# Kernel optimization log

Measured on AMD Instinct MI355X. Metric: run time of the kernel, lower is better.

Reference implementation:

```python
import jax, jax.numpy as jnp
import numpy as np

B, T, E, S, W, H = 2, 2048, 256, 128, 8, 150

def _mlp(x, w1, b1, w2, b2, w3, b3):
    # Score module: Linear->ReLU->Linear->ReLU->Linear (dropout inactive in eval)
    h = jax.nn.relu(x @ w1 + b1)
    h = jax.nn.relu(h @ w2 + b2)
    return h @ w3 + b3

def _mlp_params(key, d_in):
    k1, k2, k3 = jax.random.split(key, 3)
    s = 0.02
    return (s * jax.random.normal(k1, (d_in, H), jnp.float32), jnp.zeros((H,), jnp.float32),
            s * jax.random.normal(k2, (H, H), jnp.float32), jnp.zeros((H,), jnp.float32),
            s * jax.random.normal(k3, (H, 1), jnp.float32), jnp.zeros((1,), jnp.float32))

def setup_inputs() -> dict:
    key = jax.random.key(0)
    ke, ks, ka, km, kp = jax.random.split(key, 5)
    inp = {
        'batch_embeds': jax.random.normal(ke, (B, T, E), jnp.float32),
        'span_starts': jax.random.randint(ks, (B, S), 0, T - W, jnp.int32),
    }
    for name, k, d in [('attn', ka, E), ('ment', km, 3 * E), ('pair', kp, 9 * E)]:
        w1, b1, w2, b2, w3, b3 = _mlp_params(k, d)
        inp.update({f'{name}_w1': w1, f'{name}_b1': b1, f'{name}_w2': w2,
                    f'{name}_b2': b2, f'{name}_w3': w3, f'{name}_b3': b3})
    return inp

def reference(batch_embeds, span_starts,
              attn_w1, attn_b1, attn_w2, attn_b2, attn_w3, attn_b3,
              ment_w1, ment_b1, ment_w2, ment_b2, ment_w3, ment_b3,
              pair_w1, pair_b1, pair_w2, pair_b2, pair_w3, pair_b3):
    # ---- MentionScore ----
    attns = _mlp(batch_embeds, attn_w1, attn_b1, attn_w2, attn_b2, attn_w3, attn_b3)  # [B,T,1]
    spans = span_starts[:, :, None] + jnp.arange(W)                                   # [B,S,W]
    flat = spans.reshape(B, S * W)
    emb_spans = jnp.take_along_axis(batch_embeds, flat[:, :, None], axis=1).reshape(B, S, W, E)
    attn_spans = jnp.take_along_axis(attns, flat[:, :, None], axis=1).reshape(B, S, W, 1)
    start = emb_spans[:, :, 0, :]
    end = emb_spans[:, :, -1, :]
    weighted = jnp.sum(emb_spans * attn_spans, axis=2)                                # [B,S,E]
    g_i = jnp.concatenate([start, end, weighted], axis=-1)                            # [B,S,3E]
    mention_scores = _mlp(g_i, ment_w1, ment_b1, ment_w2, ment_b2, ment_w3, ment_b3)  # [B,S,1]
    # ---- PairwiseScore: all-pairs cat(g_i, g_j, g_i*g_j) ----
    gi = jnp.broadcast_to(g_i[:, :, None, :], (B, S, S, 3 * E))
    gj = jnp.broadcast_to(g_i[:, None, :, :], (B, S, S, 3 * E))
    pairs = jnp.concatenate([gi, gj, gi * gj], axis=-1)                               # [B,S,S,9E]
    pair_scores = _mlp(pairs, pair_w1, pair_b1, pair_w2, pair_b2, pair_w3, pair_b3)   # [B,S,S,1]
    # extended score = mean(mention_i, mention_j, pair_ij)
    ext = (mention_scores[:, :, None, :] + mention_scores[:, None, :, :] + pair_scores) / 3.0
    return ext
```

## Files before the change

### kernel.cpp

```cpp
#include <hip/hip_runtime.h>
#include <hip/hip_bf16.h>


typedef __bf16 bf16;
typedef __attribute__((ext_vector_type(8))) short v8s;
typedef __attribute__((ext_vector_type(8))) __bf16 v8bf;
typedef __attribute__((ext_vector_type(4))) float v4f;

#define MFMA_BF16(A, B, C) __builtin_amdgcn_mfma_f32_16x16x32_bf16((A), (B), (C), 0, 0, 0)

__device__ __forceinline__ v8bf mul_cvt8(float4 xa, float4 xb, float4 sa, float4 sb) {
    v8bf w;
    w[0] = (bf16)(xa.x * sa.x); w[1] = (bf16)(xa.y * sa.y);
    w[2] = (bf16)(xa.z * sa.z); w[3] = (bf16)(xa.w * sa.w);
    w[4] = (bf16)(xb.x * sb.x); w[5] = (bf16)(xb.y * sb.y);
    w[6] = (bf16)(xb.z * sb.z); w[7] = (bf16)(xb.w * sb.w);
    return w;
}
__device__ __forceinline__ v8bf cvt8(float4 xa, float4 xb) {
    v8bf w;
    w[0] = (bf16)xa.x; w[1] = (bf16)xa.y; w[2] = (bf16)xa.z; w[3] = (bf16)xa.w;
    w[4] = (bf16)xb.x; w[5] = (bf16)xb.y; w[6] = (bf16)xb.z; w[7] = (bf16)xb.w;
    return w;
}

__global__ __launch_bounds__(256) void prep_kernel(
    const float* __restrict__ pw1, const float* __restrict__ pw2,
    const float* __restrict__ aw1, const float* __restrict__ aw2,
    const float* __restrict__ mw1, const float* __restrict__ mw2,
    const float* __restrict__ pb1, const float* __restrict__ pb2, const float* __restrict__ pw3,
    const float* __restrict__ ab1, const float* __restrict__ ab2, const float* __restrict__ aw3,
    const float* __restrict__ mb1, const float* __restrict__ mb2, const float* __restrict__ mw3,
    bf16* __restrict__ w1cT, bf16* __restrict__ w2pT,
    bf16* __restrict__ w1aT, bf16* __restrict__ w2aT, bf16* __restrict__ w2mT,
    bf16* __restrict__ wuvmT, float* __restrict__ bias)
{
    int idx = blockIdx.x * 256 + threadIdx.x;
    if (idx < 147456) {
        int h = idx / 768, e = idx % 768;
        w1cT[idx] = (bf16)((h < 150) ? pw1[(1536 + e) * 150 + h] : 0.f);
    } else if (idx < 178176) {
        int j = idx - 147456; int n = j / 160, k = j % 160;
        w2pT[j] = (bf16)((n < 150 && k < 150) ? pw2[k * 150 + n] : 0.f);
    } else if (idx < 227328) {
        int j = idx - 178176; int h = j / 256, e = j % 256;
        w1aT[j] = (bf16)((h < 150) ? aw1[e * 150 + h] : 0.f);
    } else if (idx < 258048) {
        int j = idx - 227328; int n = j / 160, k = j % 160;
        w2aT[j] = (bf16)((n < 150 && k < 150) ? aw2[k * 150 + n] : 0.f);
    } else if (idx < 288768) {
        int j = idx - 258048; int n = j / 160, k = j % 160;
        w2mT[j] = (bf16)((n < 150 && k < 150) ? mw2[k * 150 + n] : 0.f);
    } else if (idx < 731136) {
        int j = idx - 288768; int s = j / 147456; int r = j % 147456;
        int h = r / 768, e = r % 768;
        float v = 0.f;
        if (h < 150) {
            if (s == 0)      v = pw1[e * 150 + h];
            else if (s == 1) v = pw1[(768 + e) * 150 + h];
            else             v = mw1[e * 150 + h];
        }
        wuvmT[j] = (bf16)v;
    } else if (idx < 732864) {
        int j = idx - 731136; int arr = j / 192, h = j % 192;
        const float* src;
        switch (arr) {
            case 0: src = pb1; break; case 1: src = pb2; break; case 2: src = pw3; break;
            case 3: src = ab1; break; case 4: src = ab2; break; case 5: src = aw3; break;
            case 6: src = mb1; break; case 7: src = mb2; break; default: src = mw3; break;
        }
        bias[j] = (h < 150) ? src[h] : 0.f;
    }
}

__global__ __launch_bounds__(256) void build_g_kernel(
    const float* __restrict__ emb, const int* __restrict__ spans,
    const float* __restrict__ attns, float* __restrict__ g)
{
    int blk = blockIdx.x;
    int b = blk >> 7;
    int t0 = spans[blk];
    int e = threadIdx.x;
    const float* eb = emb + ((size_t)(b * 2048 + t0)) * 256 + e;
    const float* at = attns + b * 2048 + t0;
    float start = eb[0];
    float endv  = eb[7 * 256];
    float wsum = 0.f;
#pragma unroll
    for (int w = 0; w < 8; ++w) wsum = fmaf(eb[w * 256], at[w], wsum);
    g[(size_t)blk * 768 + e]       = start;
    g[(size_t)blk * 768 + 256 + e] = endv;
    g[(size_t)blk * 768 + 512 + e] = wsum;
}

#define SMEM_BYTES 76800
#define A_ELEMS 4608
#define B_ELEMS 13824

__global__ __launch_bounds__(512) void attn_mfma_kernel(
    const float* __restrict__ emb,
    const bf16* __restrict__ w1aT, const bf16* __restrict__ w2aT,
    const float* __restrict__ b1p, const float* __restrict__ b2p,
    const float* __restrict__ w3p, const float* __restrict__ b3,
    float* __restrict__ attns)
{
    __shared__ __attribute__((aligned(16))) char smem[SMEM_BYTES];
    bf16*  a_lds  = (bf16*)smem;
    bf16*  b_lds  = (bf16*)(smem + 18432);
    bf16*  h1_lds = (bf16*)smem;
    float* red    = (float*)(smem + 22528);

    const int m0  = blockIdx.x * 64;
    const int tid = threadIdx.x;
    const int lane = tid & 63;
    const int wm = (tid >> 6) >> 2, wn = (tid >> 6) & 3;
    const int l15 = lane & 15, lk = (lane >> 4) * 8;
    const int aj = tid >> 3, ae = (tid & 7) * 8;
    const int bn = tid >> 1, bk = (tid & 1) * 32;

    {
        const float* gs = emb + (size_t)(m0 + aj) * 256 + ae;
        float4 x0 = *(const float4*)(gs + 0), x1 = *(const float4*)(gs + 4);
        *(v8bf*)(a_lds + aj * 72 + ae) = cvt8(x0, x1);
        if (tid < 384) {
            const bf16* bs = w1aT + bn * 256 + bk;
            bf16* bd = b_lds + bn * 72 + bk;
#pragma unroll
            for (int c2 = 0; c2 < 4; ++c2)
                *(uint4*)(bd + c2 * 8) = *(const uint4*)(bs + c2 * 8);
        }
    }
    __syncthreads();

    v4f acc[2][3];
#pragma unroll
    for (int mf = 0; mf < 2; ++mf)
#pragma unroll
        for (int nf = 0; nf < 3; ++nf) acc[mf][nf] = (v4f){0.f, 0.f, 0.f, 0.f};

    int cur = 0;
    for (int c = 0; c < 4; ++c) {
        float4 x0, x1;
        uint4 bv0, bv1, bv2, bv3;
        if (c < 3) {
            const int e0 = (c + 1) * 64;
            const float* gs = emb + (size_t)(m0 + aj) * 256 + e0 + ae;
            x0 = *(const float4*)(gs + 0); x1 = *(const float4*)(gs + 4);
            if (tid < 384) {
                const bf16* bs = w1aT + bn * 256 + e0 + bk;
                bv0 = *(const uint4*)(bs + 0);  bv1 = *(const uint4*)(bs + 8);
                bv2 = *(const uint4*)(bs + 16); bv3 = *(const uint4*)(bs + 24);
            }
        }
        const bf16* ab = a_lds + cur * A_ELEMS;
        const bf16* bb = b_lds + cur * B_ELEMS;
#pragma unroll
        for (int ks = 0; ks < 2; ++ks) {
            const int kb = ks * 32 + lk;
            v8s af[2], bfr[3];
#pragma unroll
            for (int mf = 0; mf < 2; ++mf)
                af[mf] = *(const v8s*)&ab[(wm * 32 + mf * 16 + l15) * 72 + kb];
#pragma unroll
            for (int nf = 0; nf < 3; ++nf)
                bfr[nf] = *(const v8s*)&bb[(wn * 48 + nf * 16 + l15) * 72 + kb];
#pragma unroll
            for (int mf = 0; mf < 2; ++mf)
#pragma unroll
                for (int nf = 0; nf < 3; ++nf)
                    acc[mf][nf] = MFMA_BF16(af[mf], bfr[nf], acc[mf][nf]);
        }
        if (c < 3) {
            *(v8bf*)(a_lds + (cur ^ 1) * A_ELEMS + aj * 72 + ae) = cvt8(x0, x1);
            if (tid < 384) {
                bf16* bd = b_lds + (cur ^ 1) * B_ELEMS + bn * 72 + bk;
                *(uint4*)(bd + 0)  = bv0; *(uint4*)(bd + 8)  = bv1;
                *(uint4*)(bd + 16) = bv2; *(uint4*)(bd + 24) = bv3;
            }
        }
        __syncthreads();
        cur ^= 1;
    }

    {
        const float b10 = b1p[wn * 48 + 0  + l15];
        const float b11 = b1p[wn * 48 + 16 + l15];
        const float b12 = b1p[wn * 48 + 32 + l15];
#pragma unroll
        for (int mf = 0; mf < 2; ++mf) {
#pragma unroll
            for (int r = 0; r < 4; ++r) {
                const int jl = wm * 32 + mf * 16 + (lane >> 4) * 4 + r;
                bf16* hrow = h1_lds + jl * 168 + wn * 48 + l15;
                hrow[0] = (bf16)fmaxf(acc[mf][0][r] + b10, 0.f);
                if (wn < 3) {
                    hrow[16] = (bf16)fmaxf(acc[mf][1][r] + b11, 0.f);
                    hrow[32] = (bf16)fmaxf(acc[mf][2][r] + b12, 0.f);
                }
            }
        }
    }
    __syncthreads();

    v4f acc2[2][3];
#pragma unroll
    for (int mf = 0; mf < 2; ++mf)
#pragma unroll
        for (int nf = 0; nf < 3; ++nf) acc2[mf][nf] = (v4f){0.f, 0.f, 0.f, 0.f};
#pragma unroll
    for (int ks = 0; ks < 5; ++ks) {
        const int kb = ks * 32 + lk;
        v8s af[2], bfr[3];
#pragma unroll
        for (int mf = 0; mf < 2; ++mf)
            af[mf] = *(const v8s*)&h1_lds[(wm * 32 + mf * 16 + l15) * 168 + kb];
#pragma unroll
        for (int nf = 0; nf < 3; ++nf)
            bfr[nf] = *(const v8s*)&w2aT[(size_t)(wn * 48 + nf * 16 + l15) * 160 + kb];
#pragma unroll
        for (int mf = 0; mf < 2; ++mf)
#pragma unroll
            for (int nf = 0; nf < 3; ++nf)
                acc2[mf][nf] = MFMA_BF16(af[mf], bfr[nf], acc2[mf][nf]);
    }

    const float b2v0 = b2p[wn * 48 + 0  + l15], w3v0 = w3p[wn * 48 + 0  + l15];
    const float b2v1 = b2p[wn * 48 + 16 + l15], w3v1 = w3p[wn * 48 + 16 + l15];
    const float b2v2 = b2p[wn * 48 + 32 + l15], w3v2 = w3p[wn * 48 + 32 + l15];
#pragma unroll
    for (int mf = 0; mf < 2; ++mf) {
#pragma unroll
        for (int r = 0; r < 4; ++r) {
            float p = fmaxf(acc2[mf][0][r] + b2v0, 0.f) * w3v0
                    + fmaxf(acc2[mf][1][r] + b2v1, 0.f) * w3v1
                    + fmaxf(acc2[mf][2][r] + b2v2, 0.f) * w3v2;
            p += __shfl_xor(p, 1);
            p += __shfl_xor(p, 2);
            p += __shfl_xor(p, 4);
            p += __shfl_xor(p, 8);
            if (l15 == 0) {
                const int jl = wm * 32 + mf * 16 + (lane >> 4) * 4 + r;
                red[jl * 4 + wn] = p;
            }
        }
    }
    __syncthreads();
    if (tid < 64) {
        attns[m0 + tid] = red[tid * 4 + 0] + red[tid * 4 + 1]
                        + red[tid * 4 + 2] + red[tid * 4 + 3] + b3[0];
    }
}

__global__ __launch_bounds__(512) void uvm_mfma_kernel(
    const float* __restrict__ g, const bf16* __restrict__ wuvmT,
    const bf16* __restrict__ w2mT,
    const float* __restrict__ pb1p, const float* __restrict__ mb1p,
    const float* __restrict__ mb2p, const float* __restrict__ mw3p,
    const float* __restrict__ mb3,
    float* __restrict__ u_pad, float* __restrict__ v_pad, float* __restrict__ ment)
{
    __shared__ __attribute__((aligned(16))) char smem[SMEM_BYTES];
    bf16*  a_lds  = (bf16*)smem;
    bf16*  b_lds  = (bf16*)(smem + 18432);
    bf16*  h1_lds = (bf16*)smem;
    float* red    = (float*)(smem + 22528);

    const int sect = blockIdx.x >> 2;
    const int m0   = (blockIdx.x & 3) * 64;
    const bf16* Bw = wuvmT + (size_t)sect * 147456;
    const int tid = threadIdx.x;
    const int lane = tid & 63;
    const int wm = (tid >> 6) >> 2, wn = (tid >> 6) & 3;
    const int l15 = lane & 15, lk = (lane >> 4) * 8;
    const int aj = tid >> 3, ae = (tid & 7) * 8;
    const int bn = tid >> 1, bk = (tid & 1) * 32;

    {
        const float* gs = g + (size_t)(m0 + aj) * 768 + ae;
        float4 x0 = *(const float4*)(gs + 0), x1 = *(const float4*)(gs + 4);
        *(v8bf*)(a_lds + aj * 72 + ae) = cvt8(x0, x1);
        if (tid < 384) {
            const bf16* bs = Bw + bn * 768 + bk;
            bf16* bd = b_lds + bn * 72 + bk;
#pragma unroll
            for (int c2 = 0; c2 < 4; ++c2)
                *(uint4*)(bd + c2 * 8) = *(const uint4*)(bs + c2 * 8);
        }
    }
    __syncthreads();

    v4f acc[2][3];
#pragma unroll
    for (int mf = 0; mf < 2; ++mf)
#pragma unroll
        for (int nf = 0; nf < 3; ++nf) acc[mf][nf] = (v4f){0.f, 0.f, 0.f, 0.f};

    int cur = 0;
    for (int c = 0; c < 12; ++c) {
        float4 x0, x1;
        uint4 bv0, bv1, bv2, bv3;
        if (c < 11) {
            const int e0 = (c + 1) * 64;
            const float* gs = g + (size_t)(m0 + aj) * 768 + e0 + ae;
            x0 = *(const float4*)(gs + 0); x1 = *(const float4*)(gs + 4);
            if (tid < 384) {
                const bf16* bs = Bw + bn * 768 + e0 + bk;
                bv0 = *(const uint4*)(bs + 0);  bv1 = *(const uint4*)(bs + 8);
                bv2 = *(const uint4*)(bs + 16); bv3 = *(const uint4*)(bs + 24);
            }
        }
        const bf16* ab = a_lds + cur * A_ELEMS;
        const bf16* bb = b_lds + cur * B_ELEMS;
#pragma unroll
        for (int ks = 0; ks < 2; ++ks) {
            const int kb = ks * 32 + lk;
            v8s af[2], bfr[3];
#pragma unroll
            for (int mf = 0; mf < 2; ++mf)
                af[mf] = *(const v8s*)&ab[(wm * 32 + mf * 16 + l15) * 72 + kb];
#pragma unroll
            for (int nf = 0; nf < 3; ++nf)
                bfr[nf] = *(const v8s*)&bb[(wn * 48 + nf * 16 + l15) * 72 + kb];
#pragma unroll
            for (int mf = 0; mf < 2; ++mf)
#pragma unroll
                for (int nf = 0; nf < 3; ++nf)
                    acc[mf][nf] = MFMA_BF16(af[mf], bfr[nf], acc[mf][nf]);
        }
        if (c < 11) {
            *(v8bf*)(a_lds + (cur ^ 1) * A_ELEMS + aj * 72 + ae) = cvt8(x0, x1);
            if (tid < 384) {
                bf16* bd = b_lds + (cur ^ 1) * B_ELEMS + bn * 72 + bk;
                *(uint4*)(bd + 0)  = bv0; *(uint4*)(bd + 8)  = bv1;
                *(uint4*)(bd + 16) = bv2; *(uint4*)(bd + 24) = bv3;
            }
        }
        __syncthreads();
        cur ^= 1;
    }

    if (sect < 2) {
        float* dst = (sect == 0) ? u_pad : v_pad;
        const float bb0 = (sect == 0) ? pb1p[wn * 48 + 0  + l15] : 0.f;
        const float bb1 = (sect == 0) ? pb1p[wn * 48 + 16 + l15] : 0.f;
        const float bb2 = (sect == 0) ? pb1p[wn * 48 + 32 + l15] : 0.f;
#pragma unroll
        for (int mf = 0; mf < 2; ++mf) {
#pragma unroll
            for (int r = 0; r < 4; ++r) {
                const int jl = wm * 32 + mf * 16 + (lane >> 4) * 4 + r;
                float* drow = dst + (size_t)(m0 + jl) * 192 + wn * 48 + l15;
                drow[0]  = acc[mf][0][r] + bb0;
                drow[16] = acc[mf][1][r] + bb1;
                drow[32] = acc[mf][2][r] + bb2;
            }
        }
        return;
    }

    {
        const float b10 = mb1p[wn * 48 + 0  + l15];
        const float b11 = mb1p[wn * 48 + 16 + l15];
        const float b12 = mb1p[wn * 48 + 32 + l15];
#pragma unroll
        for (int mf = 0; mf < 2; ++mf) {
#pragma unroll
            for (int r = 0; r < 4; ++r) {
                const int jl = wm * 32 + mf * 16 + (lane >> 4) * 4 + r;
                bf16* hrow = h1_lds + jl * 168 + wn * 48 + l15;
                hrow[0] = (bf16)fmaxf(acc[mf][0][r] + b10, 0.f);
                if (wn < 3) {
                    hrow[16] = (bf16)fmaxf(acc[mf][1][r] + b11, 0.f);
                    hrow[32] = (bf16)fmaxf(acc[mf][2][r] + b12, 0.f);
                }
            }
        }
    }
    __syncthreads();

    v4f acc2[2][3];
#pragma unroll
    for (int mf = 0; mf < 2; ++mf)
#pragma unroll
        for (int nf = 0; nf < 3; ++nf) acc2[mf][nf] = (v4f){0.f, 0.f, 0.f, 0.f};
#pragma unroll
    for (int ks = 0; ks < 5; ++ks) {
        const int kb = ks * 32 + lk;
        v8s af[2], bfr[3];
#pragma unroll
        for (int mf = 0; mf < 2; ++mf)
            af[mf] = *(const v8s*)&h1_lds[(wm * 32 + mf * 16 + l15) * 168 + kb];
#pragma unroll
        for (int nf = 0; nf < 3; ++nf)
            bfr[nf] = *(const v8s*)&w2mT[(size_t)(wn * 48 + nf * 16 + l15) * 160 + kb];
#pragma unroll
        for (int mf = 0; mf < 2; ++mf)
#pragma unroll
            for (int nf = 0; nf < 3; ++nf)
                acc2[mf][nf] = MFMA_BF16(af[mf], bfr[nf], acc2[mf][nf]);
    }

    const float b2v0 = mb2p[wn * 48 + 0  + l15], w3v0 = mw3p[wn * 48 + 0  + l15];
    const float b2v1 = mb2p[wn * 48 + 16 + l15], w3v1 = mw3p[wn * 48 + 16 + l15];
    const float b2v2 = mb2p[wn * 48 + 32 + l15], w3v2 = mw3p[wn * 48 + 32 + l15];
#pragma unroll
    for (int mf = 0; mf < 2; ++mf) {
#pragma unroll
        for (int r = 0; r < 4; ++r) {
            float p = fmaxf(acc2[mf][0][r] + b2v0, 0.f) * w3v0
                    + fmaxf(acc2[mf][1][r] + b2v1, 0.f) * w3v1
                    + fmaxf(acc2[mf][2][r] + b2v2, 0.f) * w3v2;
            p += __shfl_xor(p, 1);
            p += __shfl_xor(p, 2);
            p += __shfl_xor(p, 4);
            p += __shfl_xor(p, 8);
            if (l15 == 0) {
                const int jl = wm * 32 + mf * 16 + (lane >> 4) * 4 + r;
                red[jl * 4 + wn] = p;
            }
        }
    }
    __syncthreads();
    if (tid < 64) {
        ment[m0 + tid] = red[tid * 4 + 0] + red[tid * 4 + 1]
                       + red[tid * 4 + 2] + red[tid * 4 + 3] + mb3[0];
    }
}

__global__ __launch_bounds__(512) void pair_mfma_kernel(
    const float* __restrict__ g,
    const float* __restrict__ u_pad, const float* __restrict__ v_pad,
    const bf16* __restrict__ w1cT, const bf16* __restrict__ w2T,
    const float* __restrict__ b2_pad, const float* __restrict__ w3_pad,
    const float* __restrict__ pb3, const float* __restrict__ ment,
    float* __restrict__ out)
{
    __shared__ __attribute__((aligned(16))) char smem[SMEM_BYTES];
    bf16*  a_lds  = (bf16*)smem;
    bf16*  b_lds  = (bf16*)(smem + 18432);
    float* gi_s   = (float*)(smem + 73728);
    bf16*  h1_lds = (bf16*)smem;
    float* red    = (float*)(smem + 22528);

    const int blk   = blockIdx.x;
    const int b     = blk >> 8;
    const int i     = (blk >> 1) & 127;
    const int half  = blk & 1;
    const int row_i = b * 128 + i;
    const int jg0   = b * 128 + half * 64;
    const int tid   = threadIdx.x;
    const int lane  = tid & 63;
    const int wm = (tid >> 6) >> 2, wn = (tid >> 6) & 3;
    const int l15 = lane & 15, lk = (lane >> 4) * 8;
    const int aj = tid >> 3, ae = (tid & 7) * 8;
    const int bn = tid >> 1, bk = (tid & 1) * 32;

    if (tid < 192)
        *(float4*)&gi_s[tid * 4] = *(const float4*)&g[(size_t)row_i * 768 + tid * 4];
    __syncthreads();

    {
        const float* gs = g + (size_t)(jg0 + aj) * 768 + ae;
        float4 x0 = *(const float4*)(gs + 0), x1 = *(const float4*)(gs + 4);
        const float* gp = gi_s + ae;
        float4 s0 = *(const float4*)(gp + 0), s1 = *(const float4*)(gp + 4);
        *(v8bf*)(a_lds + aj * 72 + ae) = mul_cvt8(x0, x1, s0, s1);
        if (tid < 384) {
            const bf16* bs = w1cT + bn * 768 + bk;
            bf16* bd = b_lds + bn * 72 + bk;
#pragma unroll
            for (int c2 = 0; c2 < 4; ++c2)
                *(uint4*)(bd + c2 * 8) = *(const uint4*)(bs + c2 * 8);
        }
    }
    __syncthreads();

    v4f acc[2][3];
#pragma unroll
    for (int mf = 0; mf < 2; ++mf)
#pragma unroll
        for (int nf = 0; nf < 3; ++nf) acc[mf][nf] = (v4f){0.f, 0.f, 0.f, 0.f};

    int cur = 0;
    for (int c = 0; c < 12; ++c) {
        float4 x0, x1;
        uint4 bv0, bv1, bv2, bv3;
        if (c < 11) {
            const int e0 = (c + 1) * 64;
            const float* gs = g + (size_t)(jg0 + aj) * 768 + e0 + ae;
            x0 = *(const float4*)(gs + 0); x1 = *(const float4*)(gs + 4);
            if (tid < 384) {
                const bf16* bs = w1cT + bn * 768 + e0 + bk;
                bv0 = *(const uint4*)(bs + 0);  bv1 = *(const uint4*)(bs + 8);
                bv2 = *(const uint4*)(bs + 16); bv3 = *(const uint4*)(bs + 24);
            }
        }
        const bf16* ab = a_lds + cur * A_ELEMS;
        const bf16* bb = b_lds + cur * B_ELEMS;
#pragma unroll
        for (int ks = 0; ks < 2; ++ks) {
            const int kb = ks * 32 + lk;
            v8s af[2], bfr[3];
#pragma unroll
            for (int mf = 0; mf < 2; ++mf)
                af[mf] = *(const v8s*)&ab[(wm * 32 + mf * 16 + l15) * 72 + kb];
#pragma unroll
            for (int nf = 0; nf < 3; ++nf)
                bfr[nf] = *(const v8s*)&bb[(wn * 48 + nf * 16 + l15) * 72 + kb];
#pragma unroll
            for (int mf = 0; mf < 2; ++mf)
#pragma unroll
                for (int nf = 0; nf < 3; ++nf)
                    acc[mf][nf] = MFMA_BF16(af[mf], bfr[nf], acc[mf][nf]);
        }
        if (c < 11) {
            const float* gp = gi_s + (c + 1) * 64 + ae;
            float4 s0 = *(const float4*)(gp + 0), s1 = *(const float4*)(gp + 4);
            *(v8bf*)(a_lds + (cur ^ 1) * A_ELEMS + aj * 72 + ae) = mul_cvt8(x0, x1, s0, s1);
            if (tid < 384) {
                bf16* bd = b_lds + (cur ^ 1) * B_ELEMS + bn * 72 + bk;
                *(uint4*)(bd + 0)  = bv0; *(uint4*)(bd + 8)  = bv1;
                *(uint4*)(bd + 16) = bv2; *(uint4*)(bd + 24) = bv3;
            }
        }
        __syncthreads();
        cur ^= 1;
    }

    {
        const float uh0 = u_pad[row_i * 192 + wn * 48 + 0  + l15];
        const float uh1 = u_pad[row_i * 192 + wn * 48 + 16 + l15];
        const float uh2 = u_pad[row_i * 192 + wn * 48 + 32 + l15];
#pragma unroll
        for (int mf = 0; mf < 2; ++mf) {
#pragma unroll
            for (int r = 0; r < 4; ++r) {
                const int jl = wm * 32 + mf * 16 + (lane >> 4) * 4 + r;
                const float* vrow = v_pad + (size_t)(jg0 + jl) * 192 + wn * 48 + l15;
                const float v0 = acc[mf][0][r] + uh0 + vrow[0];
                const float v1 = acc[mf][1][r] + uh1 + vrow[16];
                const float v2 = acc[mf][2][r] + uh2 + vrow[32];
                bf16* hrow = h1_lds + jl * 168 + wn * 48 + l15;
                hrow[0] = (bf16)fmaxf(v0, 0.f);
                if (wn < 3) {
                    hrow[16] = (bf16)fmaxf(v1, 0.f);
                    hrow[32] = (bf16)fmaxf(v2, 0.f);
                }
            }
        }
    }
    __syncthreads();

    v4f acc2[2][3];
#pragma unroll
    for (int mf = 0; mf < 2; ++mf)
#pragma unroll
        for (int nf = 0; nf < 3; ++nf) acc2[mf][nf] = (v4f){0.f, 0.f, 0.f, 0.f};
#pragma unroll
    for (int ks = 0; ks < 5; ++ks) {
        const int kb = ks * 32 + lk;
        v8s af[2], bfr[3];
#pragma unroll
        for (int mf = 0; mf < 2; ++mf)
            af[mf] = *(const v8s*)&h1_lds[(wm * 32 + mf * 16 + l15) * 168 + kb];
#pragma unroll
        for (int nf = 0; nf < 3; ++nf)
            bfr[nf] = *(const v8s*)&w2T[(size_t)(wn * 48 + nf * 16 + l15) * 160 + kb];
#pragma unroll
        for (int mf = 0; mf < 2; ++mf)
#pragma unroll
            for (int nf = 0; nf < 3; ++nf)
                acc2[mf][nf] = MFMA_BF16(af[mf], bfr[nf], acc2[mf][nf]);
    }

    const float b2v0 = b2_pad[wn * 48 + 0  + l15], w3v0 = w3_pad[wn * 48 + 0  + l15];
    const float b2v1 = b2_pad[wn * 48 + 16 + l15], w3v1 = w3_pad[wn * 48 + 16 + l15];
    const float b2v2 = b2_pad[wn * 48 + 32 + l15], w3v2 = w3_pad[wn * 48 + 32 + l15];
#pragma unroll
    for (int mf = 0; mf < 2; ++mf) {
#pragma unroll
        for (int r = 0; r < 4; ++r) {
            float p = fmaxf(acc2[mf][0][r] + b2v0, 0.f) * w3v0
                    + fmaxf(acc2[mf][1][r] + b2v1, 0.f) * w3v1
                    + fmaxf(acc2[mf][2][r] + b2v2, 0.f) * w3v2;
            p += __shfl_xor(p, 1);
            p += __shfl_xor(p, 2);
            p += __shfl_xor(p, 4);
            p += __shfl_xor(p, 8);
            if (l15 == 0) {
                const int jl = wm * 32 + mf * 16 + (lane >> 4) * 4 + r;
                red[jl * 4 + wn] = p;
            }
        }
    }
    __syncthreads();
    if (tid < 64) {
        const float s = red[tid * 4 + 0] + red[tid * 4 + 1] + red[tid * 4 + 2] + red[tid * 4 + 3];
        out[(size_t)b * 16384 + (size_t)i * 128 + half * 64 + tid] =
            (s + pb3[0] + ment[row_i] + ment[b * 128 + half * 64 + tid]) * (1.f / 3.f);
    }
}

extern "C" void kernel_launch(void* const* d_in, const int* in_sizes, int n_in,
                              void* d_out, int out_size, void* d_ws, size_t ws_size,
                              hipStream_t stream)
{
    const float* emb   = (const float*)d_in[0];
    const int*   spans = (const int*)d_in[1];
    const float* aw1 = (const float*)d_in[2];
    const float* ab1 = (const float*)d_in[3];
    const float* aw2 = (const float*)d_in[4];
    const float* ab2 = (const float*)d_in[5];
    const float* aw3 = (const float*)d_in[6];
    const float* ab3 = (const float*)d_in[7];
    const float* mw1 = (const float*)d_in[8];
    const float* mb1 = (const float*)d_in[9];
    const float* mw2 = (const float*)d_in[10];
    const float* mb2 = (const float*)d_in[11];
    const float* mw3 = (const float*)d_in[12];
    const float* mb3 = (const float*)d_in[13];
    const float* pw1 = (const float*)d_in[14];
    const float* pb1 = (const float*)d_in[15];
    const float* pw2 = (const float*)d_in[16];
    const float* pb2 = (const float*)d_in[17];
    const float* pw3 = (const float*)d_in[18];
    const float* pb3 = (const float*)d_in[19];

    float* ws    = (float*)d_ws;
    float* attns = ws;
    float* g     = ws + 4096;
    float* ment  = ws + 200704;
    float* u_pad = ws + 200960;
    float* v_pad = ws + 250112;
    float* bias  = ws + 299264;
    float* pb1p = bias;         float* pb2p = bias + 192;  float* pw3p = bias + 384;
    float* ab1p = bias + 576;   float* ab2p = bias + 768;  float* aw3p = bias + 960;
    float* mb1p = bias + 1152;  float* mb2p = bias + 1344; float* mw3p = bias + 1536;
    bf16* w1cT  = (bf16*)(ws + 300992);
    bf16* w2pT  = (bf16*)(ws + 374720);
    bf16* w1aT  = (bf16*)(ws + 390080);
    bf16* w2aT  = (bf16*)(ws + 414656);
    bf16* w2mT  = (bf16*)(ws + 430016);
    bf16* wuvmT = (bf16*)(ws + 445376);

    prep_kernel<<<2863, 256, 0, stream>>>(pw1, pw2, aw1, aw2, mw1, mw2,
                                          pb1, pb2, pw3, ab1, ab2, aw3, mb1, mb2, mw3,
                                          w1cT, w2pT, w1aT, w2aT, w2mT, wuvmT, bias);
    attn_mfma_kernel<<<64, 512, 0, stream>>>(emb, w1aT, w2aT, ab1p, ab2p, aw3p, ab3, attns);
    build_g_kernel<<<256, 256, 0, stream>>>(emb, spans, attns, g);
    uvm_mfma_kernel<<<12, 512, 0, stream>>>(g, wuvmT, w2mT, pb1p, mb1p, mb2p, mw3p, mb3,
                                            u_pad, v_pad, ment);
    pair_mfma_kernel<<<512, 512, 0, stream>>>(g, u_pad, v_pad, w1cT, w2pT,
                                              pb2p, pw3p, pb3, ment, (float*)d_out);
}
```

Baseline: 65.62 us.

## Halve M tile in attn/uvm kernels and deepen global prefetch to two stages

The attention and mention/uv MLP kernels now use 32-row M tiles, which doubles their grid sizes to 128 and 24 blocks so more CUs are busy on these small launches. All three MFMA kernels switch to a two-deep register prefetch of the A and B chunks, with the K loop fully unrolled. Weight loading is also spread across all 512 threads. The cost is more register pressure, and the B weight tile is loaded twice as often per row of output in the smaller-tile kernels.

After: 105.8 us. 1.61x slower.

```diff
diff --git a/kernel.cpp b/kernel.cpp
--- a/kernel.cpp
+++ b/kernel.cpp
@@ -93,93 +93,93 @@
     g[(size_t)blk * 768 + 512 + e] = wsum;
 }
 
-#define SMEM_BYTES 76800
-#define A_ELEMS 4608
-#define B_ELEMS 13824
-
-__global__ __launch_bounds__(512) void attn_mfma_kernel(
+#define A32_ELEMS 2304
+#define B_ELEMS   13824
+
+__global__ __launch_bounds__(512, 4) void attn_mfma_kernel(
     const float* __restrict__ emb,
     const bf16* __restrict__ w1aT, const bf16* __restrict__ w2aT,
     const float* __restrict__ b1p, const float* __restrict__ b2p,
     const float* __restrict__ w3p, const float* __restrict__ b3,
     float* __restrict__ attns)
 {
-    __shared__ __attribute__((aligned(16))) char smem[SMEM_BYTES];
+    __shared__ __attribute__((aligned(16))) char smem[64512];
     bf16*  a_lds  = (bf16*)smem;
-    bf16*  b_lds  = (bf16*)(smem + 18432);
+    bf16*  b_lds  = (bf16*)(smem + 9216);
     bf16*  h1_lds = (bf16*)smem;
-    float* red    = (float*)(smem + 22528);
-
-    const int m0  = blockIdx.x * 64;
+    float* red    = (float*)(smem + 10752);
+
+    const int m0  = blockIdx.x * 32;
     const int tid = threadIdx.x;
     const int lane = tid & 63;
     const int wm = (tid >> 6) >> 2, wn = (tid >> 6) & 3;
     const int l15 = lane & 15, lk = (lane >> 4) * 8;
     const int aj = tid >> 3, ae = (tid & 7) * 8;
-    const int bn = tid >> 1, bk = (tid & 1) * 32;
-
-    {
-        const float* gs = emb + (size_t)(m0 + aj) * 256 + ae;
-        float4 x0 = *(const float4*)(gs + 0), x1 = *(const float4*)(gs + 4);
-        *(v8bf*)(a_lds + aj * 72 + ae) = cvt8(x0, x1);
-        if (tid < 384) {
-            const bf16* bs = w1aT + bn * 256 + bk;
-            bf16* bd = b_lds + bn * 72 + bk;
-#pragma unroll
-            for (int c2 = 0; c2 < 4; ++c2)
-                *(uint4*)(bd + c2 * 8) = *(const uint4*)(bs + c2 * 8);
-        }
-    }
-    __syncthreads();
-
-    v4f acc[2][3];
-#pragma unroll
-    for (int mf = 0; mf < 2; ++mf)
-#pragma unroll
-        for (int nf = 0; nf < 3; ++nf) acc[mf][nf] = (v4f){0.f, 0.f, 0.f, 0.f};
-
-    int cur = 0;
+    const float* gA = emb + (size_t)(m0 + aj) * 256 + ae;
+
+    {
+        if (tid < 256) {
+            float4 x0 = *(const float4*)(gA + 0), x1 = *(const float4*)(gA + 4);
+            *(v8bf*)(a_lds + aj * 72 + ae) = cvt8(x0, x1);
+        }
+#pragma unroll
+        for (int s2 = 0; s2 < 3; ++s2) {
+            const int li = tid + s2 * 512, row = li >> 3, c8 = (li & 7) * 8;
+            *(uint4*)(b_lds + row * 72 + c8) = *(const uint4*)(w1aT + row * 256 + c8);
+        }
+    }
+    float4 xq[2][2];
+    uint4  bq[2][3];
+    {
+        if (tid < 256) { xq[1][0] = *(const float4*)(gA + 64); xq[1][1] = *(const float4*)(gA + 68); }
+#pragma unroll
+        for (int s2 = 0; s2 < 3; ++s2) {
+            const int li = tid + s2 * 512, row = li >> 3, c8 = (li & 7) * 8;
+            bq[1][s2] = *(const uint4*)(w1aT + row * 256 + 64 + c8);
+        }
+    }
+    __syncthreads();
+
+    v4f acc[3];
+#pragma unroll
+    for (int nf = 0; nf < 3; ++nf) acc[nf] = (v4f){0.f, 0.f, 0.f, 0.f};
+
+#pragma unroll
     for (int c = 0; c < 4; ++c) {
-        float4 x0, x1;
-        uint4 bv0, bv1, bv2, bv3;
-        if (c < 3) {
-            const int e0 = (c + 1) * 64;
-            const float* gs = emb + (size_t)(m0 + aj) * 256 + e0 + ae;
-            x0 = *(const float4*)(gs + 0); x1 = *(const float4*)(gs + 4);
-            if (tid < 384) {
-                const bf16* bs = w1aT + bn * 256 + e0 + bk;
-                bv0 = *(const uint4*)(bs + 0);  bv1 = *(const uint4*)(bs + 8);
-                bv2 = *(const uint4*)(bs + 16); bv3 = *(const uint4*)(bs + 24);
-            }
-        }
-        const bf16* ab = a_lds + cur * A_ELEMS;
-        const bf16* bb = b_lds + cur * B_ELEMS;
+        if (c + 2 < 4) {
+            const int e0 = (c + 2) * 64;
+            if (tid < 256) { xq[c & 1][0] = *(const float4*)(gA + e0); xq[c & 1][1] = *(const float4*)(gA + e0 + 4); }
+#pragma unroll
+            for (int s2 = 0; s2 < 3; ++s2) {
+                const int li = tid + s2 * 512, row = li >> 3, c8 = (li & 7) * 8;
+                bq[c & 1][s2] = *(const uint4*)(w1aT + row * 256 + e0 + c8);
+            }
+        }
+        const bf16* ab = a_lds + (c & 1) * A32_ELEMS;
+        const bf16* bb = b_lds + (c & 1) * B_ELEMS;
 #pragma unroll
         for (int ks = 0; ks < 2; ++ks) {
             const int kb = ks * 32 + lk;
-            v8s af[2], bfr[3];
-#pragma unroll
-            for (int mf = 0; mf < 2; ++mf)
-                af[mf] = *(const v8s*)&ab[(wm * 32 + mf * 16 + l15) * 72 + kb];
+            v8s af = *(const v8s*)&ab[(wm * 16 + l15) * 72 + kb];
+            v8s bfr[3];
 #pragma unroll
             for (int nf = 0; nf < 3; ++nf)
                 bfr[nf] = *(const v8s*)&bb[(wn * 48 + nf * 16 + l15) * 72 + kb];
 #pragma unroll
-            for (int mf = 0; mf < 2; ++mf)
-#pragma unroll
-                for (int nf = 0; nf < 3; ++nf)
-                    acc[mf][nf] = MFMA_BF16(af[mf], bfr[nf], acc[mf][nf]);
-        }
-        if (c < 3) {
-            *(v8bf*)(a_lds + (cur ^ 1) * A_ELEMS + aj * 72 + ae) = cvt8(x0, x1);
-            if (tid < 384) {
-                bf16* bd = b_lds + (cur ^ 1) * B_ELEMS + bn * 72 + bk;
-                *(uint4*)(bd + 0)  = bv0; *(uint4*)(bd + 8)  = bv1;
-                *(uint4*)(bd + 16) = bv2; *(uint4*)(bd + 24) = bv3;
+            for (int nf = 0; nf < 3; ++nf)
+                acc[nf] = MFMA_BF16(af, bfr[nf], acc[nf]);
+        }
+        if (c + 1 < 4) {
+            const int p = (c & 1) ^ 1;
+            if (tid < 256)
+                *(v8bf*)(a_lds + ((c + 1) & 1) * A32_ELEMS + aj * 72 + ae) = cvt8(xq[p][0], xq[p][1]);
+#pragma unroll
+            for (int s2 = 0; s2 < 3; ++s2) {
+                const int li = tid + s2 * 512, row = li >> 3, c8 = (li & 7) * 8;
+                *(uint4*)(b_lds + ((c + 1) & 1) * B_ELEMS + row * 72 + c8) = bq[p][s2];
             }
         }
         __syncthreads();
-        cur ^= 1;
     }
 
     {
@@ -187,71 +187,59 @@
         const float b11 = b1p[wn * 48 + 16 + l15];
         const float b12 = b1p[wn * 48 + 32 + l15];
 #pragma unroll
-        for (int mf = 0; mf < 2; ++mf) {
-#pragma unroll
-            for (int r = 0; r < 4; ++r) {
-                const int jl = wm * 32 + mf * 16 + (lane >> 4) * 4 + r;
-                bf16* hrow = h1_lds + jl * 168 + wn * 48 + l15;
-                hrow[0] = (bf16)fmaxf(acc[mf][0][r] + b10, 0.f);
-                if (wn < 3) {
-                    hrow[16] = (bf16)fmaxf(acc[mf][1][r] + b11, 0.f);
-                    hrow[32] = (bf16)fmaxf(acc[mf][2][r] + b12, 0.f);
-                }
-            }
-        }
-    }
-    __syncthreads();
-
-    v4f acc2[2][3];
-#pragma unroll
-    for (int mf = 0; mf < 2; ++mf)
-#pragma unroll
-        for (int nf = 0; nf < 3; ++nf) acc2[mf][nf] = (v4f){0.f, 0.f, 0.f, 0.f};
+        for (int r = 0; r < 4; ++r) {
+            const int jl = wm * 16 + (lane >> 4) * 4 + r;
+            bf16* hrow = h1_lds + jl * 168 + wn * 48 + l15;
+            hrow[0] = (bf16)fmaxf(acc[0][r] + b10, 0.f);
+            if (wn < 3) {
+                hrow[16] = (bf16)fmaxf(acc[1][r] + b11, 0.f);
+                hrow[32] = (bf16)fmaxf(acc[2][r] + b12, 0.f);
+            }
+        }
+    }
+    __syncthreads();
+
+    v4f acc2[3];
+#pragma unroll
+    for (int nf = 0; nf < 3; ++nf) acc2[nf] = (v4f){0.f, 0.f, 0.f, 0.f};
 #pragma unroll
     for (int ks = 0; ks < 5; ++ks) {
         const int kb = ks * 32 + lk;
-        v8s af[2], bfr[3];
-#pragma unroll
-        for (int mf = 0; mf < 2; ++mf)
-            af[mf] = *(const v8s*)&h1_lds[(wm * 32 + mf * 16 + l15) * 168 + kb];
+        v8s af = *(const v8s*)&h1_lds[(wm * 16 + l15) * 168 + kb];
+        v8s bfr[3];
 #pragma unroll
         for (int nf = 0; nf < 3; ++nf)
             bfr[nf] = *(const v8s*)&w2aT[(size_t)(wn * 48 + nf * 16 + l15) * 160 + kb];
 #pragma unroll
-        for (int mf = 0; mf < 2; ++mf)
-#pragma unroll
-            for (int nf = 0; nf < 3; ++nf)
-                acc2[mf][nf] = MFMA_BF16(af[mf], bfr[nf], acc2[mf][nf]);
+        for (int nf = 0; nf < 3; ++nf)
+            acc2[nf] = MFMA_BF16(af, bfr[nf], acc2[nf]);
     }
 
     const float b2v0 = b2p[wn * 48 + 0  + l15], w3v0 = w3p[wn * 48 + 0  + l15];
     const float b2v1 = b2p[wn * 48 + 16 + l15], w3v1 = w3p[wn * 48 + 16 + l15];
     const float b2v2 = b2p[wn * 48 + 32 + l15], w3v2 = w3p[wn * 48 + 32 + l15];
 #pragma unroll
-    for (int mf = 0; mf < 2; ++mf) {
-#pragma unroll
-        for (int r = 0; r < 4; ++r) {
-            float p = fmaxf(acc2[mf][0][r] + b2v0, 0.f) * w3v0
-                    + fmaxf(acc2[mf][1][r] + b2v1, 0.f) * w3v1
-                    + fmaxf(acc2[mf][2][r] + b2v2, 0.f) * w3v2;
-            p += __shfl_xor(p, 1);
-            p += __shfl_xor(p, 2);
-            p += __shfl_xor(p, 4);
-            p += __shfl_xor(p, 8);
-            if (l15 == 0) {
-                const int jl = wm * 32 + mf * 16 + (lane >> 4) * 4 + r;
-                red[jl * 4 + wn] = p;
-            }
-        }
-    }
-    __syncthreads();
-    if (tid < 64) {
+    for (int r = 0; r < 4; ++r) {
+        float p = fmaxf(acc2[0][r] + b2v0, 0.f) * w3v0
+                + fmaxf(acc2[1][r] + b2v1, 0.f) * w3v1
+                + fmaxf(acc2[2][r] + b2v2, 0.f) * w3v2;
+        p += __shfl_xor(p, 1);
+        p += __shfl_xor(p, 2);
+        p += __shfl_xor(p, 4);
+        p += __shfl_xor(p, 8);
+        if (l15 == 0) {
+            const int jl = wm * 16 + (lane >> 4) * 4 + r;
+            red[jl * 4 + wn] = p;
+        }
+    }
+    __syncthreads();
+    if (tid < 32) {
         attns[m0 + tid] = red[tid * 4 + 0] + red[tid * 4 + 1]
                         + red[tid * 4 + 2] + red[tid * 4 + 3] + b3[0];
     }
 }
 
-__global__ __launch_bounds__(512) void uvm_mfma_kernel(
+__global__ __launch_bounds__(512, 4) void uvm_mfma_kernel(
     const float* __restrict__ g, const bf16* __restrict__ wuvmT,
     const bf16* __restrict__ w2mT,
     const float* __restrict__ pb1p, const float* __restrict__ mb1p,
@@ -259,84 +247,85 @@
     const float* __restrict__ mb3,
     float* __restrict__ u_pad, float* __restrict__ v_pad, float* __restrict__ ment)
 {
-    __shared__ __attribute__((aligned(16))) char smem[SMEM_BYTES];
+    __shared__ __attribute__((aligned(16))) char smem[64512];
     bf16*  a_lds  = (bf16*)smem;
-    bf16*  b_lds  = (bf16*)(smem + 18432);
+    bf16*  b_lds  = (bf16*)(smem + 9216);
     bf16*  h1_lds = (bf16*)smem;
-    float* red    = (float*)(smem + 22528);
-
-    const int sect = blockIdx.x >> 2;
-    const int m0   = (blockIdx.x & 3) * 64;
+    float* red    = (float*)(smem + 10752);
+
+    const int sect = blockIdx.x >> 3;
+    const int m0   = (blockIdx.x & 7) * 32;
     const bf16* Bw = wuvmT + (size_t)sect * 147456;
     const int tid = threadIdx.x;
     const int lane = tid & 63;
     const int wm = (tid >> 6) >> 2, wn = (tid >> 6) & 3;
     const int l15 = lane & 15, lk = (lane >> 4) * 8;
     const int aj = tid >> 3, ae = (tid & 7) * 8;
-    const int bn = tid >> 1, bk = (tid & 1) * 32;
-
-    {
-        const float* gs = g + (size_t)(m0 + aj) * 768 + ae;
-        float4 x0 = *(const float4*)(gs + 0), x1 = *(const float4*)(gs + 4);
-        *(v8bf*)(a_lds + aj * 72 + ae) = cvt8(x0, x1);
-        if (tid < 384) {
-            const bf16* bs = Bw + bn * 768 + bk;
-            bf16* bd = b_lds + bn * 72 + bk;
-#pragma unroll
-            for (int c2 = 0; c2 < 4; ++c2)
-                *(uint4*)(bd + c2 * 8) = *(const uint4*)(bs + c2 * 8);
-        }
-    }
-    __syncthreads();
-
-    v4f acc[2][3];
-#pragma unroll
-    for (int mf = 0; mf < 2; ++mf)
-#pragma unroll
-        for (int nf = 0; nf < 3; ++nf) acc[mf][nf] = (v4f){0.f, 0.f, 0.f, 0.f};
-
-    int cur = 0;
+    const float* gA = g + (size_t)(m0 + aj) * 768 + ae;
+
+    {
+        if (tid < 256) {
+            float4 x0 = *(const float4*)(gA + 0), x1 = *(const float4*)(gA + 4);
+            *(v8bf*)(a_lds + aj * 72 + ae) = cvt8(x0, x1);
+        }
+#pragma unroll
+        for (int s2 = 0; s2 < 3; ++s2) {
+            const int li = tid + s2 * 512, row = li >> 3, c8 = (li & 7) * 8;
+            *(uint4*)(b_lds + row * 72 + c8) = *(const uint4*)(Bw + row * 768 + c8);
+        }
+    }
+    float4 xq[2][2];
+    uint4  bq[2][3];
+    {
+        if (tid < 256) { xq[1][0] = *(const float4*)(gA + 64); xq[1][1] = *(const float4*)(gA + 68); }
+#pragma unroll
+        for (int s2 = 0; s2 < 3; ++s2) {
+            const int li = tid + s2 * 512, row = li >> 3, c8 = (li & 7) * 8;
+            bq[1][s2] = *(const uint4*)(Bw + row * 768 + 64 + c8);
+        }
+    }
+    __syncthreads();
+
+    v4f acc[3];
+#pragma unroll
+    for (int nf = 0; nf < 3; ++nf) acc[nf] = (v4f){0.f, 0.f, 0.f, 0.f};
+
+#pragma unroll
     for (int c = 0; c < 12; ++c) {
-        float4 x0, x1;
-        uint4 bv0, bv1, bv2, bv3;
-        if (c < 11) {
-            const int e0 = (c + 1) * 64;
-            const float* gs = g + (size_t)(m0 + aj) * 768 + e0 + ae;
-            x0 = *(const float4*)(gs + 0); x1 = *(const float4*)(gs + 4);
-            if (tid < 384) {
-                const bf16* bs = Bw + bn * 768 + e0 + bk;
-                bv0 = *(const uint4*)(bs + 0);  bv1 = *(const uint4*)(bs + 8);
-                bv2 = *(const uint4*)(bs + 16); bv3 = *(const uint4*)(bs + 24);
-            }
-        }
-        const bf16* ab = a_lds + cur * A_ELEMS;
-        const bf16* bb = b_lds + cur * B_ELEMS;
+        if (c + 2 < 12) {
+            const int e0 = (c + 2) * 64;
+            if (tid < 256) { xq[c & 1][0] = *(const float4*)(gA + e0); xq[c & 1][1] = *(const float4*)(gA + e0 + 4); }
+#pragma unroll
+            for (int s2 = 0; s2 < 3; ++s2) {
+                const int li = tid + s2 * 512, row = li >> 3, c8 = (li & 7) * 8;
+                bq[c & 1][s2] = *(const uint4*)(Bw + row * 768 + e0 + c8);
+            }
+        }
+        const bf16* ab = a_lds + (c & 1) * A32_ELEMS;
+        const bf16* bb = b_lds + (c & 1) * B_ELEMS;
 #pragma unroll
         for (int ks = 0; ks < 2; ++ks) {
             const int kb = ks * 32 + lk;
-            v8s af[2], bfr[3];
-#pragma unroll
-            for (int mf = 0; mf < 2; ++mf)
-                af[mf] = *(const v8s*)&ab[(wm * 32 + mf * 16 + l15) * 72 + kb];
+            v8s af = *(const v8s*)&ab[(wm * 16 + l15) * 72 + kb];
+            v8s bfr[3];
 #pragma unroll
             for (int nf = 0; nf < 3; ++nf)
                 bfr[nf] = *(const v8s*)&bb[(wn * 48 + nf * 16 + l15) * 72 + kb];
 #pragma unroll
-            for (int mf = 0; mf < 2; ++mf)
-#pragma unroll
-                for (int nf = 0; nf < 3; ++nf)
-                    acc[mf][nf] = MFMA_BF16(af[mf], bfr[nf], acc[mf][nf]);
-        }
-        if (c < 11) {
-            *(v8bf*)(a_lds + (cur ^ 1) * A_ELEMS + aj * 72 + ae) = cvt8(x0, x1);
-            if (tid < 384) {
-                bf16* bd = b_lds + (cur ^ 1) * B_ELEMS + bn * 72 + bk;
-                *(uint4*)(bd + 0)  = bv0; *(uint4*)(bd + 8)  = bv1;
-                *(uint4*)(bd + 16) = bv2; *(uint4*)(bd + 24) = bv3;
+            for (int nf = 0; nf < 3; ++nf)
+                acc[nf] = MFMA_BF16(af, bfr[nf], acc[nf]);
+        }
+        if (c + 1 < 12) {
+            const int p = (c & 1) ^ 1;
+            if (tid < 256)
+                *(v8bf*)(a_lds + ((c + 1) & 1) * A32_ELEMS + aj * 72 + ae) = cvt8(xq[p][0], xq[p][1]);
+#pragma unroll
+            for (int s2 = 0; s2 < 3; ++s2) {
+                const int li = tid + s2 * 512, row = li >> 3, c8 = (li & 7) * 8;
+                *(uint4*)(b_lds + ((c + 1) & 1) * B_ELEMS + row * 72 + c8) = bq[p][s2];
             }
         }
         __syncthreads();
-        cur ^= 1;
     }
 
     if (sect < 2) {
@@ -345,15 +334,12 @@
         const float bb1 = (sect == 0) ? pb1p[wn * 48 + 16 + l15] : 0.f;
         const float bb2 = (sect == 0) ? pb1p[wn * 48 + 32 + l15] : 0.f;
 #pragma unroll
-        for (int mf = 0; mf < 2; ++mf) {
-#pragma unroll
-            for (int r = 0; r < 4; ++r) {
-                const int jl = wm * 32 + mf * 16 + (lane >> 4) * 4 + r;
-                float* drow = dst + (size_t)(m0 + jl) * 192 + wn * 48 + l15;
-                drow[0]  = acc[mf][0][r] + bb0;
-                drow[16] = acc[mf][1][r] + bb1;
-                drow[32] = acc[mf][2][r] + bb2;
-            }
+        for (int r = 0; r < 4; ++r) {
+            const int jl = wm * 16 + (lane >> 4) * 4 + r;
+            float* drow = dst + (size_t)(m0 + jl) * 192 + wn * 48 + l15;
+            drow[0]  = acc[0][r] + bb0;
+            drow[16] = acc[1][r] + bb1;
+            drow[32] = acc[2][r] + bb2;
         }
         return;
     }
@@ -363,71 +349,60 @@
         const float b11 = mb1p[wn * 48 + 16 + l15];
         const float b12 = mb1p[wn * 48 + 32 + l15];
 #pragma unroll
-        for (int mf = 0; mf < 2; ++mf) {
-#pragma unroll
-            for (int r = 0; r < 4; ++r) {
-                const int jl = wm * 32 + mf * 16 + (lane >> 4) * 4 + r;
-                bf16* hrow = h1_lds + jl * 168 + wn * 48 + l15;
-                hrow[0] = (bf16)fmaxf(acc[mf][0][r] + b10, 0.f);
-                if (wn < 3) {
-                    hrow[16] = (bf16)fmaxf(acc[mf][1][r] + b11, 0.f);
-                    hrow[32] = (bf16)fmaxf(acc[mf][2][r] + b12, 0.f);
-                }
-            }
-        }
-    }
-    __syncthreads();
-
-    v4f acc2[2][3];
-#pragma unroll
-    for (int mf = 0; mf < 2; ++mf)
-#pragma unroll
-        for (int nf = 0; nf < 3; ++nf) acc2[mf][nf] = (v4f){0.f, 0.f, 0.f, 0.f};
+        for (int r = 0; r < 4; ++r) {
+            const int jl = wm * 16 + (lane >> 4) * 4 + r;
+            bf16* hrow = h1_lds + jl * 168 + wn * 48 + l15;
+            hrow[0] = (bf16)fmaxf(acc[0][r] + b10, 0.f);
+            if (wn < 3) {
+                hrow[16] = (bf16)fmaxf(acc[1][r] + b11, 0.f);
+                hrow[32] = (bf16)fmaxf(acc[2][r] + b12, 0.f);
+            }
+        }
+    }
+    __syncthreads();
+
+    v4f acc2[3];
+#pragma unroll
+    for (int nf = 0; nf < 3; ++nf) acc2[nf] = (v4f){0.f, 0.f, 0.f, 0.f};
 #pragma unroll
     for (int ks = 0; ks < 5; ++ks) {
         const int kb = ks * 32 + lk;
-        v8s af[2], bfr[3];
-#pragma unroll
-        for (int mf = 0; mf < 2; ++mf)
-            af[mf] = *(const v8s*)&h1_lds[(wm * 32 + mf * 16 + l15) * 168 + kb];
+        v8s af = *(const v8s*)&h1_lds[(wm * 16 + l15) * 168 + kb];
+        v8s bfr[3];
 #pragma unroll
         for (int nf = 0; nf < 3; ++nf)
             bfr[nf] = *(const v8s*)&w2mT[(size_t)(wn * 48 + nf * 16 + l15) * 160 + kb];
 #pragma unroll
-        for (int mf = 0; mf < 2; ++mf)
-#pragma unroll
-            for (int nf = 0; nf < 3; ++nf)
-                acc2[mf][nf] = MFMA_BF16(af[mf], bfr[nf], acc2[mf][nf]);
+        for (int nf = 0; nf < 3; ++nf)
+            acc2[nf] = MFMA_BF16(af, bfr[nf], acc2[nf]);
     }
 
     const float b2v0 = mb2p[wn * 48 + 0  + l15], w3v0 = mw3p[wn * 48 + 0  + l15];
     const float b2v1 = mb2p[wn * 48 + 16 + l15], w3v1 = mw3p[wn * 48 + 16 + l15];
     const float b2v2 = mb2p[wn * 48 + 32 + l15], w3v2 = mw3p[wn * 48 + 32 + l15];
 #pragma unroll
-    for (int mf = 0; mf < 2; ++mf) {
-#pragma unroll
-        for (int r = 0; r < 4; ++r) {
-            float p = fmaxf(acc2[mf][0][r] + b2v0, 0.f) * w3v0
-                    + fmaxf(acc2[mf][1][r] + b2v1, 0.f) * w3v1
-                    + fmaxf(acc2[mf][2][r] + b2v2, 0.f) * w3v2;
-            p += __shfl_xor(p, 1);
-            p += __shfl_xor(p, 2);
-            p += __shfl_xor(p, 4);
-            p += __shfl_xor(p, 8);
-            if (l15 == 0) {
-                const int jl = wm * 32 + mf * 16 + (lane >> 4) * 4 + r;
-                red[jl * 4 + wn] = p;
-            }
-        }
-    }
-    __syncthreads();
-    if (tid < 64) {
+    for (int r = 0; r < 4; ++r) {
+        float p = fmaxf(acc2[0][r] + b2v0, 0.f) * w3v0
+                + fmaxf(acc2[1][r] + b2v1, 0.f) * w3v1
+                + fmaxf(acc2[2][r] + b2v2, 0.f) * w3v2;
+        p += __shfl_xor(p, 1);
+        p += __shfl_xor(p, 2);
+        p += __shfl_xor(p, 4);
+        p += __shfl_xor(p, 8);
+        if (l15 == 0) {
+            const int jl = wm * 16 + (lane >> 4) * 4 + r;
+            red[jl * 4 + wn] = p;
+        }
+    }
+    __syncthreads();
+    if (tid < 32) {
         ment[m0 + tid] = red[tid * 4 + 0] + red[tid * 4 + 1]
                        + red[tid * 4 + 2] + red[tid * 4 + 3] + mb3[0];
     }
 }
 
-__global__ __launch_bounds__(512) void pair_mfma_kernel(
+#define A64_ELEMS 4608
+__global__ __launch_bounds__(512, 4) void pair_mfma_kernel(
     const float* __restrict__ g,
     const float* __restrict__ u_pad, const float* __restrict__ v_pad,
     const bf16* __restrict__ w1cT, const bf16* __restrict__ w2T,
@@ -435,42 +410,50 @@
     const float* __restrict__ pb3, const float* __restrict__ ment,
     float* __restrict__ out)
 {
-    __shared__ __attribute__((aligned(16))) char smem[SMEM_BYTES];
+    __shared__ __attribute__((aligned(16))) char smem[76800];
     bf16*  a_lds  = (bf16*)smem;
     bf16*  b_lds  = (bf16*)(smem + 18432);
     float* gi_s   = (float*)(smem + 73728);
     bf16*  h1_lds = (bf16*)smem;
     float* red    = (float*)(smem + 22528);
 
-    const int blk   = blockIdx.x;
-    const int b     = blk >> 8;
-    const int i     = (blk >> 1) & 127;
-    const int half  = blk & 1;
+    const int blk = blockIdx.x;
+    const int b = blk >> 8;
+    const int i = (blk >> 1) & 127;
+    const int half = blk & 1;
     const int row_i = b * 128 + i;
-    const int jg0   = b * 128 + half * 64;
-    const int tid   = threadIdx.x;
-    const int lane  = tid & 63;
+    const int jg0 = b * 128 + half * 64;
+    const int tid = threadIdx.x;
+    const int lane = tid & 63;
     const int wm = (tid >> 6) >> 2, wn = (tid >> 6) & 3;
     const int l15 = lane & 15, lk = (lane >> 4) * 8;
     const int aj = tid >> 3, ae = (tid & 7) * 8;
-    const int bn = tid >> 1, bk = (tid & 1) * 32;
+    const float* gA = g + (size_t)(jg0 + aj) * 768 + ae;
 
     if (tid < 192)
         *(float4*)&gi_s[tid * 4] = *(const float4*)&g[(size_t)row_i * 768 + tid * 4];
     __syncthreads();
 
     {
-        const float* gs = g + (size_t)(jg0 + aj) * 768 + ae;
-        float4 x0 = *(const float4*)(gs + 0), x1 = *(const float4*)(gs + 4);
+        float4 x0 = *(const float4*)(gA + 0), x1 = *(const float4*)(gA + 4);
         const float* gp = gi_s + ae;
         float4 s0 = *(const float4*)(gp + 0), s1 = *(const float4*)(gp + 4);
         *(v8bf*)(a_lds + aj * 72 + ae) = mul_cvt8(x0, x1, s0, s1);
-        if (tid < 384) {
-            const bf16* bs = w1cT + bn * 768 + bk;
-            bf16* bd = b_lds + bn * 72 + bk;
-#pragma unroll
-            for (int c2 = 0; c2 < 4; ++c2)
-                *(uint4*)(bd + c2 * 8) = *(const uint4*)(bs + c2 * 8);
+#pragma unroll
+        for (int s2 = 0; s2 < 3; ++s2) {
+            const int li = tid + s2 * 512, row = li >> 3, c8 = (li & 7) * 8;
+            *(uint4*)(b_lds + row * 72 + c8) = *(const uint4*)(w1cT + row * 768 + c8);
+        }
+    }
+    float4 xq[2][2];
+    uint4  bq[2][3];
+    {
+        xq[1][0] = *(const float4*)(gA + 64);
+        xq[1][1] = *(const float4*)(gA + 68);
+#pragma unroll
+        for (int s2 = 0; s2 < 3; ++s2) {
+            const int li = tid + s2 * 512, row = li >> 3, c8 = (li & 7) * 8;
+            bq[1][s2] = *(const uint4*)(w1cT + row * 768 + 64 + c8);
         }
     }
     __syncthreads();
@@ -481,22 +464,20 @@
 #pragma unroll
         for (int nf = 0; nf < 3; ++nf) acc[mf][nf] = (v4f){0.f, 0.f, 0.f, 0.f};
 
-    int cur = 0;
+#pragma unroll
     for (int c = 0; c < 12; ++c) {
-        float4 x0, x1;
-        uint4 bv0, bv1, bv2, bv3;
-        if (c < 11) {
-            const int e0 = (c + 1) * 64;
-            const float* gs = g + (size_t)(jg0 + aj) * 768 + e0 + ae;
-            x0 = *(const float4*)(gs + 0); x1 = *(const float4*)(gs + 4);
-            if (tid < 384) {
-                const bf16* bs = w1cT + bn * 768 + e0 + bk;
-                bv0 = *(const uint4*)(bs + 0);  bv1 = *(const uint4*)(bs + 8);
-                bv2 = *(const uint4*)(bs + 16); bv3 = *(const uint4*)(bs + 24);
-            }
-        }
-        const bf16* ab = a_lds + cur * A_ELEMS;
-        const bf16* bb = b_lds + cur * B_ELEMS;
+        if (c + 2 < 12) {
+            const int e0 = (c + 2) * 64;
+            xq[c & 1][0] = *(const float4*)(gA + e0);
+            xq[c & 1][1] = *(const float4*)(gA + e0 + 4);
+#pragma unroll
+            for (int s2 = 0; s2 < 3; ++s2) {
+                const int li = tid + s2 * 512, row = li >> 3, c8 = (li & 7) * 8;
+                bq[c & 1][s2] = *(const uint4*)(w1cT + row * 768 + e0 + c8);
+            }
+        }
+        const bf16* ab = a_lds + (c & 1) * A64_ELEMS;
+        const bf16* bb = b_lds + (c & 1) * B_ELEMS;
 #pragma unroll
         for (int ks = 0; ks < 2; ++ks) {
             const int kb = ks * 32 + lk;
@@ -513,18 +494,19 @@
                 for (int nf = 0; nf < 3; ++nf)
                     acc[mf][nf] = MFMA_BF16(af[mf], bfr[nf], acc[mf][nf]);
         }
-        if (c < 11) {
+        if (c + 1 < 12) {
+            const int p = (c & 1) ^ 1;
             const float* gp = gi_s + (c + 1) * 64 + ae;
             float4 s0 = *(const float4*)(gp + 0), s1 = *(const float4*)(gp + 4);
-            *(v8bf*)(a_lds + (cur ^ 1) * A_ELEMS + aj * 72 + ae) = mul_cvt8(x0, x1, s0, s1);
-            if (tid < 384) {
-                bf16* bd = b_lds + (cur ^ 1) * B_ELEMS + bn * 72 + bk;
-                *(uint4*)(bd + 0)  = bv0; *(uint4*)(bd + 8)  = bv1;
-                *(uint4*)(bd + 16) = bv2; *(uint4*)(bd + 24) = bv3;
+            *(v8bf*)(a_lds + ((c + 1) & 1) * A64_ELEMS + aj * 72 + ae) =
+                mul_cvt8(xq[p][0], xq[p][1], s0, s1);
+#pragma unroll
+            for (int s2 = 0; s2 < 3; ++s2) {
+                const int li = tid + s2 * 512, row = li >> 3, c8 = (li & 7) * 8;
+                *(uint4*)(b_lds + ((c + 1) & 1) * B_ELEMS + row * 72 + c8) = bq[p][s2];
             }
         }
         __syncthreads();
-        cur ^= 1;
     }
 
     {
@@ -646,9 +628,9 @@
     prep_kernel<<<2863, 256, 0, stream>>>(pw1, pw2, aw1, aw2, mw1, mw2,
                                           pb1, pb2, pw3, ab1, ab2, aw3, mb1, mb2, mw3,
                                           w1cT, w2pT, w1aT, w2aT, w2mT, wuvmT, bias);
-    attn_mfma_kernel<<<64, 512, 0, stream>>>(emb, w1aT, w2aT, ab1p, ab2p, aw3p, ab3, attns);
+    attn_mfma_kernel<<<128, 512, 0, stream>>>(emb, w1aT, w2aT, ab1p, ab2p, aw3p, ab3, attns);
     build_g_kernel<<<256, 256, 0, stream>>>(emb, spans, attns, g);
-    uvm_mfma_kernel<<<12, 512, 0, stream>>>(g, wuvmT, w2mT, pb1p, mb1p, mb2p, mw3p, mb3,
+    uvm_mfma_kernel<<<24, 512, 0, stream>>>(g, wuvmT, w2mT, pb1p, mb1p, mb2p, mw3p, mb3,
                                             u_pad, v_pad, ment);
     pair_mfma_kernel<<<512, 512, 0, stream>>>(g, u_pad, v_pad, w1cT, w2pT,
                                               pb2p, pw3p, pb3, ment, (float*)d_out);
```
